# Performance work log

Measured on AMD Instinct MI355X. Metric: run time of the kernel, lower is better.

## Reference

```python
import jax, jax.numpy as jnp
import numpy as np

NUM_HEADS = 16


def trinity_mask(txt_tok, img_tok):
    """Boolean [N, N] mask, True = attend. Faithful to get_mask(..., 'trinity'):
    - image rows attend block-diagonally within 3 equal image chunks
    - text rows attend to all image tokens and causally to text tokens.
    """
    assert img_tok % 3 == 0, "Invalid text token sizes"
    sit = img_tok // 3
    N = txt_tok + img_tok
    i = jnp.arange(N)[:, None]
    j = jnp.arange(N)[None, :]
    img_img = (i < img_tok) & (j < img_tok) & ((i // sit) == (j // sit))
    txt_img = (i >= img_tok) & (j < img_tok)
    txt_txt = (i >= img_tok) & (j >= img_tok) & (i >= j)
    return img_img | txt_img | txt_txt


def setup_inputs() -> dict:
    key = jax.random.key(0)
    ks = jax.random.split(key, 12)
    B, TXT, IMG = 4, 512, 1536
    N = TXT + IMG
    DQ, DKV = 1024, 1024
    s = lambda d: 1.0 / np.sqrt(d).astype(np.float32)
    return {
        "q": jax.random.normal(ks[0], (B, N, DQ), jnp.float32),
        "kv": jax.random.normal(ks[1], (B, N, DKV), jnp.float32),
        "Wq": jax.random.normal(ks[2], (DQ, DQ), jnp.float32) * s(DQ),
        "bq": jnp.zeros((DQ,), jnp.float32),
        "Wk": jax.random.normal(ks[3], (DKV, DQ), jnp.float32) * s(DKV),
        "bk": jnp.zeros((DQ,), jnp.float32),
        "Wv": jax.random.normal(ks[4], (DKV, DQ), jnp.float32) * s(DKV),
        "bv": jnp.zeros((DQ,), jnp.float32),
        "Wo": jax.random.normal(ks[5], (DQ, DQ), jnp.float32) * s(DQ),
        "bo": jnp.zeros((DQ,), jnp.float32),
        "txt_tok_len": TXT,
        "img_tok_len": IMG,
    }


def reference(q, kv, Wq, bq, Wk, bk, Wv, bv, Wo, bo, txt_tok_len, img_tok_len):
    B, N, C = q.shape
    H = NUM_HEADS
    d = C // H
    scale = d ** -0.5
    # projections, split heads: [B, H, N, d]
    qh = (q @ Wq + bq).reshape(B, N, H, d).transpose(0, 2, 1, 3)
    kh = (kv @ Wk + bk).reshape(B, N, H, d).transpose(0, 2, 1, 3)
    vh = (kv @ Wv + bv).reshape(B, N, H, d).transpose(0, 2, 1, 3)
    scores = jnp.einsum("bhqd,bhkd->bhqk", qh, kh) * scale
    mask = trinity_mask(txt_tok_len, img_tok_len)  # [N, N] bool
    scores = jnp.where(mask[None, None], scores, -jnp.inf)
    attn = jax.nn.softmax(scores, axis=-1)
    # dropout in eval mode -> identity
    out = jnp.einsum("bhqk,bhkd->bhqd", attn, vh)
    out = out.transpose(0, 2, 1, 3).reshape(B, N, C)
    return out @ Wo + bo
```

## Files before the change

kernel.cpp:

```cpp
#include <hip/hip_runtime.h>


typedef _Float16 h16;
typedef _Float16 f16x8 __attribute__((ext_vector_type(8)));
typedef __fp16 fp16v2 __attribute__((ext_vector_type(2)));
typedef float f32x4 __attribute__((ext_vector_type(4)));

#define BATCH 4
#define NTOK  2048
#define CDIM  1024
#define NHEAD 16
#define HDIM  64
#define IMGTOK 1536
#define MROWS (BATCH * NTOK)
#define QSCALE 0.18033688011112042f

__device__ __forceinline__ void gload_lds16(const void* g, void* l) {
  __builtin_amdgcn_global_load_lds(
      (const __attribute__((address_space(1))) unsigned int*)g,
      (__attribute__((address_space(3))) unsigned int*)l, 16, 0, 0);
}

__global__ __launch_bounds__(256)
void cvt_f16(const float* __restrict__ s, h16* __restrict__ d) {
  size_t i = ((size_t)blockIdx.x * 256 + threadIdx.x) * 8;
  float4 a = *(const float4*)(s + i);
  float4 b = *(const float4*)(s + i + 4);
  f16x8 o;
  o[0] = (h16)a.x; o[1] = (h16)a.y; o[2] = (h16)a.z; o[3] = (h16)a.w;
  o[4] = (h16)b.x; o[5] = (h16)b.y; o[6] = (h16)b.z; o[7] = (h16)b.w;
  *(f16x8*)(d + i) = o;
}

__global__ __launch_bounds__(256)
void wtrans(const float* __restrict__ W0, const float* __restrict__ W1,
            const float* __restrict__ W2, const float* __restrict__ W3,
            h16* __restrict__ T0, h16* __restrict__ T1,
            h16* __restrict__ T2, h16* __restrict__ T3) {
  const float* W; h16* T;
  switch (blockIdx.z) {
    case 0: W = W0; T = T0; break;
    case 1: W = W1; T = T1; break;
    case 2: W = W2; T = T2; break;
    default: W = W3; T = T3; break;
  }
  __shared__ float t[32][33];
  const int n0 = blockIdx.x * 32, k0 = blockIdx.y * 32;
  const int tx = threadIdx.x, ty = threadIdx.y;
#pragma unroll
  for (int i = 0; i < 4; i++)
    t[ty + 8 * i][tx] = W[(size_t)(k0 + ty + 8 * i) * CDIM + n0 + tx];
  __syncthreads();
#pragma unroll
  for (int i = 0; i < 4; i++)
    T[(size_t)(n0 + ty + 8 * i) * CDIM + k0 + tx] = (h16)t[tx][ty + 8 * i];
}

template <int MODE>
__global__ __launch_bounds__(256, 3)
void gemm_bt(const h16* __restrict__ X, const h16* __restrict__ WT,
             const float* __restrict__ bias, void* __restrict__ outp) {
  __shared__ __attribute__((aligned(16))) h16 smem[3 * 8192];
  const int tid = threadIdx.x;
  const int lane = tid & 63;
  const int w = tid >> 6;
  const int wr = w >> 1, wc = w & 1;
  const int l15 = lane & 15, lhi = lane >> 4;
  const int m0 = blockIdx.y * 128;
  const int n0 = blockIdx.x * 128;

  f32x4 acc[4][4] = {};

  const int sr = tid >> 2;
  const int pc = tid & 3;
  const int lc = pc ^ ((sr >> 1) & 3);
  const h16* gA0 = X + (size_t)(m0 + sr) * CDIM + lc * 8;
  const h16* gA1 = gA0 + (size_t)64 * CDIM;
  const h16* gB0 = WT + (size_t)(n0 + sr) * CDIM + lc * 8;
  const h16* gB1 = gB0 + (size_t)64 * CDIM;

#define GSTAGE(bi, kt)                                      \
  do {                                                      \
    h16* A_ = smem + (bi) * 8192;                           \
    h16* B_ = A_ + 4096;                                    \
    gload_lds16(gA0 + (kt) * 32, A_ + tid * 8);             \
    gload_lds16(gA1 + (kt) * 32, A_ + (256 + tid) * 8);     \
    gload_lds16(gB0 + (kt) * 32, B_ + tid * 8);             \
    gload_lds16(gB1 + (kt) * 32, B_ + (256 + tid) * 8);     \
  } while (0)

  const int NT = CDIM / 32;
  GSTAGE(0, 0);
  GSTAGE(1, 1);
  const int rswz = (l15 >> 1) & 3;

  int rb = 0, sb = 2;
  for (int kt = 0; kt < NT; ++kt) {
    if (kt + 1 < NT) asm volatile("s_waitcnt vmcnt(4)" ::: "memory");
    else             asm volatile("s_waitcnt vmcnt(0)" ::: "memory");
    __builtin_amdgcn_s_barrier();
    if (kt + 2 < NT) { GSTAGE(sb, kt + 2); sb = (sb == 2) ? 0 : sb + 1; }
    const h16* A_ = smem + rb * 8192;
    const h16* B_ = A_ + 4096;
    rb = (rb == 2) ? 0 : rb + 1;
    f16x8 a[4], bb[4];
#pragma unroll
    for (int i = 0; i < 4; i++)
      a[i] = *(const f16x8*)(A_ + (wr * 64 + i * 16 + l15) * 32 + (lhi ^ rswz) * 8);
#pragma unroll
    for (int i = 0; i < 4; i++)
      bb[i] = *(const f16x8*)(B_ + (wc * 64 + i * 16 + l15) * 32 + (lhi ^ rswz) * 8);
    __builtin_amdgcn_s_setprio(1);
#pragma unroll
    for (int i = 0; i < 4; i++)
#pragma unroll
      for (int j = 0; j < 4; j++)
        acc[i][j] = __builtin_amdgcn_mfma_f32_16x16x32_f16(a[i], bb[j], acc[i][j], 0, 0, 0);
    __builtin_amdgcn_s_setprio(0);
  }
#undef GSTAGE

  if constexpr (MODE == 2) {
    __builtin_amdgcn_s_barrier();
    h16* T = smem;
#pragma unroll
    for (int j = 0; j < 4; j++) {
      const int gcL = wc * 64 + j * 16 + l15;
      const float bval = bias[n0 + gcL];
#pragma unroll
      for (int i = 0; i < 4; i++) {
#pragma unroll
        for (int r = 0; r < 4; r++) {
          const int grL = wr * 64 + i * 16 + lhi * 4 + r;
          const int ch = (grL >> 3) ^ (gcL & 15);
          T[gcL * 128 + ch * 8 + (grL & 7)] = (h16)(acc[i][j][r] + bval);
        }
      }
    }
    __builtin_amdgcn_s_barrier();
    const int bsel = m0 >> 11;
    const int nbase = m0 & (NTOK - 1);
    h16* outh = (h16*)outp;
#pragma unroll
    for (int pass = 0; pass < 8; ++pass) {
      const int rowL = pass * 16 + (tid >> 4);
      const int c = tid & 15;
      const int gc = n0 + rowL;
      const int hh = gc >> 6, dd = gc & 63;
      f16x8 v = *(const f16x8*)(T + rowL * 128 + ((c ^ (rowL & 15)) * 8));
      *(f16x8*)(outh + (((size_t)(bsel * NHEAD + hh)) * HDIM + dd) * NTOK +
                nbase + c * 8) = v;
    }
    return;
  }

#pragma unroll
  for (int j = 0; j < 4; j++) {
    const int gc = n0 + wc * 64 + j * 16 + l15;
    const float bval = bias[gc];
#pragma unroll
    for (int i = 0; i < 4; i++) {
      const int grb = m0 + wr * 64 + i * 16 + lhi * 4;
#pragma unroll
      for (int r = 0; r < 4; r++) {
        float v = acc[i][j][r] + bval;
        if constexpr (MODE == 3) v *= QSCALE;
        const int gr = grb + r;
        if constexpr (MODE == 0) {
          ((float*)outp)[(size_t)gr * CDIM + gc] = v;
        } else {
          const int bidx = gr >> 11, n = gr & (NTOK - 1);
          const int hh = gc >> 6, dd = gc & 63;
          ((h16*)outp)[(((size_t)(bidx * NHEAD + hh)) * NTOK + n) * HDIM + dd] = (h16)v;
        }
      }
    }
  }
}

__global__ __launch_bounds__(256)
void attn_kernel(const h16* __restrict__ Qh, const h16* __restrict__ Kh,
                 const h16* __restrict__ VTh, h16* __restrict__ AX) {
  __shared__ __attribute__((aligned(16))) h16 Kb[2][64 * 64];
  __shared__ __attribute__((aligned(16))) h16 Vb[2][64 * 64];
  __shared__ __attribute__((aligned(16))) h16 Pl[4][16 * 64];

  const int tid = threadIdx.x;
  const int lane = tid & 63;
  const int w = tid >> 6;
  const int l15 = lane & 15, lhi = lane >> 4;
  const int lhi4 = lhi * 4;

  const int id = blockIdx.x;
  const int pos = id >> 3;
  const int bh = (id & 7) * 8 + (pos >> 5);
  const int qblk = 31 - (pos & 31);
  const int b = bh >> 4, h = bh & 15;
  const int q0 = qblk * 64;

  const h16* qbase = Qh + (size_t)bh * NTOK * HDIM;
  const h16* kbase = Kh + (size_t)bh * NTOK * HDIM;
  const h16* vbase = VTh + (size_t)bh * HDIM * NTOK;

  const int qrow = q0 + w * 16 + l15;
  const f16x8 qf0 = *(const f16x8*)(qbase + (size_t)qrow * HDIM + lhi * 8);
  const f16x8 qf1 = *(const f16x8*)(qbase + (size_t)qrow * HDIM + 32 + lhi * 8);
  const int qg = qrow;

  const bool is_img = (q0 < IMGTOK);
  int kstart, kend;
  if (is_img) { kstart = q0 & ~511; kend = kstart + 512; }
  else        { kstart = 0;         kend = q0 + 64; }
  const int nt = (kend - kstart) >> 6;

  float m = -3.0e38f, lp = 0.f;
  f32x4 o[4] = {};

  const int srow = tid >> 3;
  const int scc = (tid & 7) ^ (srow & 7);
#define ASTAGE(bufi, k0s)                                                     \
  do {                                                                        \
    gload_lds16(kbase + (size_t)((k0s) + srow) * HDIM + scc * 8,              \
                Kb[bufi] + tid * 8);                                          \
    gload_lds16(kbase + (size_t)((k0s) + 32 + srow) * HDIM + scc * 8,         \
                Kb[bufi] + (256 + tid) * 8);                                  \
    gload_lds16(vbase + (size_t)srow * NTOK + (k0s) + scc * 8,                \
                Vb[bufi] + tid * 8);                                          \
    gload_lds16(vbase + (size_t)(32 + srow) * NTOK + (k0s) + scc * 8,         \
                Vb[bufi] + (256 + tid) * 8);                                  \
  } while (0)

  h16* pl = &Pl[w][0];
  const int x0 = (lhi ^ (l15 & 7)) * 8;
  const int x1 = ((lhi + 4) ^ (l15 & 7)) * 8;
  const int pswz = l15 & 7;
  const int phalf = (lhi & 1) * 4;
  const int plhi2 = lhi >> 1;
  h16* prb = pl + l15 * 64;

  ASTAGE(0, kstart);
  asm volatile("s_waitcnt vmcnt(0)" ::: "memory");
  __builtin_amdgcn_s_barrier();
  int cur = 0;

  for (int t = 0; t < nt; ++t) {
    const int k0 = kstart + t * 64;
    if (t + 1 < nt) ASTAGE(cur ^ 1, kstart + (t + 1) * 64);

    const h16* Kc = Kb[cur];
    f32x4 s[4];
    __builtin_amdgcn_s_setprio(1);
#pragma unroll
    for (int hk = 0; hk < 4; ++hk) {
      const h16* kr = Kc + (hk * 16 + l15) * 64;
      const f16x8 kfa = *(const f16x8*)(kr + x0);
      const f16x8 kfb = *(const f16x8*)(kr + x1);
      f32x4 acc = {};
      acc = __builtin_amdgcn_mfma_f32_16x16x32_f16(kfa, qf0, acc, 0, 0, 0);
      acc = __builtin_amdgcn_mfma_f32_16x16x32_f16(kfb, qf1, acc, 0, 0, 0);
      s[hk] = acc;
    }
    __builtin_amdgcn_s_setprio(0);

    const bool need_mask = (!is_img) && (k0 + 63 >= IMGTOK);
    float sv[4][4];
    float lmax = -3.0e38f;
#pragma unroll
    for (int hk = 0; hk < 4; ++hk) {
#pragma unroll
      for (int r = 0; r < 4; ++r) {
        float v = s[hk][r];
        if (need_mask) {
          const int kg = k0 + hk * 16 + lhi4 + r;
          if (kg >= IMGTOK && kg > qg) v = -1e30f;
        }
        sv[hk][r] = v;
        lmax = fmaxf(lmax, v);
      }
    }
    if (__any(lmax > m + 8.0f)) {
      float vmax = fmaxf(lmax, __shfl_xor(lmax, 16));
      vmax = fmaxf(vmax, __shfl_xor(vmax, 32));
      const float mnew = fmaxf(m, vmax);
      const float corr = exp2f(m - mnew);
      m = mnew;
      lp *= corr;
      const float c0 = __shfl(corr, lhi4 + 0);
      const float c1 = __shfl(corr, lhi4 + 1);
      const float c2 = __shfl(corr, lhi4 + 2);
      const float c3 = __shfl(corr, lhi4 + 3);
#pragma unroll
      for (int dt = 0; dt < 4; dt++) {
        o[dt][0] *= c0; o[dt][1] *= c1; o[dt][2] *= c2; o[dt][3] *= c3;
      }
    }
#pragma unroll
    for (int hk = 0; hk < 4; ++hk) {
      const float e0 = exp2f(sv[hk][0] - m);
      const float e1 = exp2f(sv[hk][1] - m);
      const float e2 = exp2f(sv[hk][2] - m);
      const float e3 = exp2f(sv[hk][3] - m);
      lp += (e0 + e1) + (e2 + e3);
      const fp16v2 lo2 = __builtin_amdgcn_cvt_pkrtz(e0, e1);
      const fp16v2 hi2 = __builtin_amdgcn_cvt_pkrtz(e2, e3);
      uint2 qw;
      qw.x = __builtin_bit_cast(unsigned int, lo2);
      qw.y = __builtin_bit_cast(unsigned int, hi2);
      *(uint2*)(prb + ((hk * 2 + plhi2) ^ pswz) * 8 + phalf) = qw;
    }
    asm volatile("s_waitcnt lgkmcnt(0)" ::: "memory");
    __builtin_amdgcn_sched_barrier(0);

    const h16* Vc = Vb[cur];
    const f16x8 pf0 = *(const f16x8*)(pl + l15 * 64 + x0);
    const f16x8 pf1 = *(const f16x8*)(pl + l15 * 64 + x1);
    __builtin_amdgcn_s_setprio(1);
#pragma unroll
    for (int dt = 0; dt < 4; dt++) {
      const h16* vr = Vc + (dt * 16 + l15) * 64;
      const f16x8 vfa = *(const f16x8*)(vr + x0);
      const f16x8 vfb = *(const f16x8*)(vr + x1);
      o[dt] = __builtin_amdgcn_mfma_f32_16x16x32_f16(pf0, vfa, o[dt], 0, 0, 0);
      o[dt] = __builtin_amdgcn_mfma_f32_16x16x32_f16(pf1, vfb, o[dt], 0, 0, 0);
    }
    __builtin_amdgcn_s_setprio(0);

    asm volatile("s_waitcnt vmcnt(0)" ::: "memory");
    __builtin_amdgcn_s_barrier();
    cur ^= 1;
  }
#undef ASTAGE

  float l = lp;
  l += __shfl_xor(l, 16);
  l += __shfl_xor(l, 32);
  const int qg0 = q0 + w * 16 + lhi4;
#pragma unroll
  for (int r = 0; r < 4; r++) {
    const float lr = __shfl(l, lhi4 + r);
    const float inv = 1.0f / lr;
    const size_t row = (size_t)(b * NTOK + qg0 + r);
#pragma unroll
    for (int dt = 0; dt < 4; dt++) {
      const int col = h * 64 + dt * 16 + l15;
      AX[row * CDIM + col] = (h16)(o[dt][r] * inv);
    }
  }
}

extern "C" void kernel_launch(void* const* d_in, const int* in_sizes, int n_in,
                              void* d_out, int out_size, void* d_ws, size_t ws_size,
                              hipStream_t stream) {
  (void)in_sizes; (void)n_in; (void)out_size; (void)ws_size;
  const float* q  = (const float*)d_in[0];
  const float* kv = (const float*)d_in[1];
  const float* Wq = (const float*)d_in[2];
  const float* bq = (const float*)d_in[3];
  const float* Wk = (const float*)d_in[4];
  const float* bk = (const float*)d_in[5];
  const float* Wv = (const float*)d_in[6];
  const float* bv = (const float*)d_in[7];
  const float* Wo = (const float*)d_in[8];
  const float* bo = (const float*)d_in[9];
  float* out = (float*)d_out;

  char* ws = (char*)d_ws;
  const size_t SZ_MK = (size_t)MROWS * CDIM * sizeof(h16);
  const size_t SZ_W  = (size_t)CDIM * CDIM * sizeof(h16);
  h16* qb  = (h16*)(ws);
  h16* kvb = (h16*)(ws + SZ_MK);
  h16* wqt = (h16*)(ws + 2 * SZ_MK);
  h16* wkt = (h16*)(ws + 2 * SZ_MK + SZ_W);
  h16* wvt = (h16*)(ws + 2 * SZ_MK + 2 * SZ_W);
  h16* wot = (h16*)(ws + 2 * SZ_MK + 3 * SZ_W);
  h16* Qh  = (h16*)(ws + 2 * SZ_MK + 4 * SZ_W);
  h16* Kh  = (h16*)(ws + 3 * SZ_MK + 4 * SZ_W);
  h16* VTh = (h16*)(ws + 4 * SZ_MK + 4 * SZ_W);
  h16* ax  = (h16*)(ws);

  cvt_f16<<<4096, 256, 0, stream>>>(q, qb);
  cvt_f16<<<4096, 256, 0, stream>>>(kv, kvb);
  wtrans<<<dim3(32, 32, 4), dim3(32, 8), 0, stream>>>(Wq, Wk, Wv, Wo,
                                                      wqt, wkt, wvt, wot);
  gemm_bt<3><<<dim3(8, 64), 256, 0, stream>>>(qb, wqt, bq, (void*)Qh);
  gemm_bt<1><<<dim3(8, 64), 256, 0, stream>>>(kvb, wkt, bk, (void*)Kh);
  gemm_bt<2><<<dim3(8, 64), 256, 0, stream>>>(kvb, wvt, bv, (void*)VTh);
  attn_kernel<<<2048, 256, 0, stream>>>(Qh, Kh, VTh, ax);
  gemm_bt<0><<<dim3(8, 64), 256, 0, stream>>>(ax, wot, bo, (void*)out);
}
```

Baseline: 329.1 us.

## Merge QKV projections into one launch and widen attention blocks to 128 queries

```diff
diff --git a/kernel.cpp b/kernel.cpp
--- a/kernel.cpp
+++ b/kernel.cpp
@@ -56,18 +56,31 @@
     T[(size_t)(n0 + ty + 8 * i) * CDIM + k0 + tx] = (h16)t[tx][ty + 8 * i];
 }
 
-template <int MODE>
+
 __global__ __launch_bounds__(256, 3)
-void gemm_bt(const h16* __restrict__ X, const h16* __restrict__ WT,
-             const float* __restrict__ bias, void* __restrict__ outp) {
+void gemm_qkv(const h16* __restrict__ qb, const h16* __restrict__ kvb,
+              const h16* __restrict__ wqt, const h16* __restrict__ wkt,
+              const h16* __restrict__ wvt,
+              const float* __restrict__ bq, const float* __restrict__ bk,
+              const float* __restrict__ bv,
+              h16* __restrict__ Qh, h16* __restrict__ Kh,
+              h16* __restrict__ VTh) {
   __shared__ __attribute__((aligned(16))) h16 smem[3 * 8192];
+  const int id = blockIdx.x;
+  const int gid = (id & 7) * 192 + (id >> 3);
+  const int which = gid >> 9;
+  const int lid = gid & 511;
+  const int m0 = (lid >> 3) * 128;
+  const int n0 = (lid & 7) * 128;
+  const h16* X  = (which == 0) ? qb : kvb;
+  const h16* WT = (which == 0) ? wqt : ((which == 1) ? wkt : wvt);
+  const float* bias = (which == 0) ? bq : ((which == 1) ? bk : bv);
+
   const int tid = threadIdx.x;
   const int lane = tid & 63;
   const int w = tid >> 6;
   const int wr = w >> 1, wc = w & 1;
   const int l15 = lane & 15, lhi = lane >> 4;
-  const int m0 = blockIdx.y * 128;
-  const int n0 = blockIdx.x * 128;
 
   f32x4 acc[4][4] = {};
 
@@ -120,7 +133,7 @@
   }
 #undef GSTAGE
 
-  if constexpr (MODE == 2) {
+  if (which == 2) {
     __builtin_amdgcn_s_barrier();
     h16* T = smem;
 #pragma unroll
@@ -140,7 +153,6 @@
     __builtin_amdgcn_s_barrier();
     const int bsel = m0 >> 11;
     const int nbase = m0 & (NTOK - 1);
-    h16* outh = (h16*)outp;
 #pragma unroll
     for (int pass = 0; pass < 8; ++pass) {
       const int rowL = pass * 16 + (tid >> 4);
@@ -148,12 +160,14 @@
       const int gc = n0 + rowL;
       const int hh = gc >> 6, dd = gc & 63;
       f16x8 v = *(const f16x8*)(T + rowL * 128 + ((c ^ (rowL & 15)) * 8));
-      *(f16x8*)(outh + (((size_t)(bsel * NHEAD + hh)) * HDIM + dd) * NTOK +
+      *(f16x8*)(VTh + (((size_t)(bsel * NHEAD + hh)) * HDIM + dd) * NTOK +
                 nbase + c * 8) = v;
     }
     return;
   }
 
+  h16* outp = (which == 0) ? Qh : Kh;
+  const float scale = (which == 0) ? QSCALE : 1.0f;
 #pragma unroll
   for (int j = 0; j < 4; j++) {
     const int gc = n0 + wc * 64 + j * 16 + l15;
@@ -163,27 +177,102 @@
       const int grb = m0 + wr * 64 + i * 16 + lhi * 4;
 #pragma unroll
       for (int r = 0; r < 4; r++) {
-        float v = acc[i][j][r] + bval;
-        if constexpr (MODE == 3) v *= QSCALE;
+        const float v = (acc[i][j][r] + bval) * scale;
         const int gr = grb + r;
-        if constexpr (MODE == 0) {
-          ((float*)outp)[(size_t)gr * CDIM + gc] = v;
-        } else {
-          const int bidx = gr >> 11, n = gr & (NTOK - 1);
-          const int hh = gc >> 6, dd = gc & 63;
-          ((h16*)outp)[(((size_t)(bidx * NHEAD + hh)) * NTOK + n) * HDIM + dd] = (h16)v;
-        }
+        const int bidx = gr >> 11, n = gr & (NTOK - 1);
+        const int hh = gc >> 6, dd = gc & 63;
+        outp[(((size_t)(bidx * NHEAD + hh)) * NTOK + n) * HDIM + dd] = (h16)v;
       }
     }
   }
 }
 
-__global__ __launch_bounds__(256)
+__global__ __launch_bounds__(256, 3)
+void gemm_out(const h16* __restrict__ X, const h16* __restrict__ WT,
+              const float* __restrict__ bias, float* __restrict__ outp) {
+  __shared__ __attribute__((aligned(16))) h16 smem[3 * 8192];
+  const int id = blockIdx.x;
+  const int gid = (id & 7) * 64 + (id >> 3);
+  const int m0 = (gid >> 3) * 128;
+  const int n0 = (gid & 7) * 128;
+
+  const int tid = threadIdx.x;
+  const int lane = tid & 63;
+  const int w = tid >> 6;
+  const int wr = w >> 1, wc = w & 1;
+  const int l15 = lane & 15, lhi = lane >> 4;
+
+  f32x4 acc[4][4] = {};
+
+  const int sr = tid >> 2;
+  const int pc = tid & 3;
+  const int lc = pc ^ ((sr >> 1) & 3);
+  const h16* gA0 = X + (size_t)(m0 + sr) * CDIM + lc * 8;
+  const h16* gA1 = gA0 + (size_t)64 * CDIM;
+  const h16* gB0 = WT + (size_t)(n0 + sr) * CDIM + lc * 8;
+  const h16* gB1 = gB0 + (size_t)64 * CDIM;
+
+#define GSTAGE(bi, kt)                                      \
+  do {                                                      \
+    h16* A_ = smem + (bi) * 8192;                           \
+    h16* B_ = A_ + 4096;                                    \
+    gload_lds16(gA0 + (kt) * 32, A_ + tid * 8);             \
+    gload_lds16(gA1 + (kt) * 32, A_ + (256 + tid) * 8);     \
+    gload_lds16(gB0 + (kt) * 32, B_ + tid * 8);             \
+    gload_lds16(gB1 + (kt) * 32, B_ + (256 + tid) * 8);     \
+  } while (0)
+
+  const int NT = CDIM / 32;
+  GSTAGE(0, 0);
+  GSTAGE(1, 1);
+  const int rswz = (l15 >> 1) & 3;
+
+  int rb = 0, sb = 2;
+  for (int kt = 0; kt < NT; ++kt) {
+    if (kt + 1 < NT) asm volatile("s_waitcnt vmcnt(4)" ::: "memory");
+    else             asm volatile("s_waitcnt vmcnt(0)" ::: "memory");
+    __builtin_amdgcn_s_barrier();
+    if (kt + 2 < NT) { GSTAGE(sb, kt + 2); sb = (sb == 2) ? 0 : sb + 1; }
+    const h16* A_ = smem + rb * 8192;
+    const h16* B_ = A_ + 4096;
+    rb = (rb == 2) ? 0 : rb + 1;
+    f16x8 a[4], bb[4];
+#pragma unroll
+    for (int i = 0; i < 4; i++)
+      a[i] = *(const f16x8*)(A_ + (wr * 64 + i * 16 + l15) * 32 + (lhi ^ rswz) * 8);
+#pragma unroll
+    for (int i = 0; i < 4; i++)
+      bb[i] = *(const f16x8*)(B_ + (wc * 64 + i * 16 + l15) * 32 + (lhi ^ rswz) * 8);
+    __builtin_amdgcn_s_setprio(1);
+#pragma unroll
+    for (int i = 0; i < 4; i++)
+#pragma unroll
+      for (int j = 0; j < 4; j++)
+        acc[i][j] = __builtin_amdgcn_mfma_f32_16x16x32_f16(a[i], bb[j], acc[i][j], 0, 0, 0);
+    __builtin_amdgcn_s_setprio(0);
+  }
+#undef GSTAGE
+
+#pragma unroll
+  for (int j = 0; j < 4; j++) {
+    const int gc = n0 + wc * 64 + j * 16 + l15;
+    const float bval = bias[gc];
+#pragma unroll
+    for (int i = 0; i < 4; i++) {
+      const int grb = m0 + wr * 64 + i * 16 + lhi * 4;
+#pragma unroll
+      for (int r = 0; r < 4; r++)
+        outp[(size_t)(grb + r) * CDIM + gc] = acc[i][j][r] + bval;
+    }
+  }
+}
+
+__global__ __launch_bounds__(512, 6)
 void attn_kernel(const h16* __restrict__ Qh, const h16* __restrict__ Kh,
                  const h16* __restrict__ VTh, h16* __restrict__ AX) {
   __shared__ __attribute__((aligned(16))) h16 Kb[2][64 * 64];
   __shared__ __attribute__((aligned(16))) h16 Vb[2][64 * 64];
-  __shared__ __attribute__((aligned(16))) h16 Pl[4][16 * 64];
+  __shared__ __attribute__((aligned(16))) h16 Pl[8][16 * 64];
 
   const int tid = threadIdx.x;
   const int lane = tid & 63;
@@ -193,10 +282,10 @@
 
   const int id = blockIdx.x;
   const int pos = id >> 3;
-  const int bh = (id & 7) * 8 + (pos >> 5);
-  const int qblk = 31 - (pos & 31);
+  const int bh = (id & 7) * 8 + (pos >> 4);
+  const int qblk = 15 - (pos & 15);
   const int b = bh >> 4, h = bh & 15;
-  const int q0 = qblk * 64;
+  const int q0 = qblk * 128;
 
   const h16* qbase = Qh + (size_t)bh * NTOK * HDIM;
   const h16* kbase = Kh + (size_t)bh * NTOK * HDIM;
@@ -208,9 +297,8 @@
   const int qg = qrow;
 
   const bool is_img = (q0 < IMGTOK);
-  int kstart, kend;
-  if (is_img) { kstart = q0 & ~511; kend = kstart + 512; }
-  else        { kstart = 0;         kend = q0 + 64; }
+  const int kstart = is_img ? (q0 & ~511) : 0;
+  const int kend = is_img ? (kstart + 512) : (q0 + 128);
   const int nt = (kend - kstart) >> 6;
 
   float m = -3.0e38f, lp = 0.f;
@@ -222,12 +310,8 @@
   do {                                                                        \
     gload_lds16(kbase + (size_t)((k0s) + srow) * HDIM + scc * 8,              \
                 Kb[bufi] + tid * 8);                                          \
-    gload_lds16(kbase + (size_t)((k0s) + 32 + srow) * HDIM + scc * 8,         \
-                Kb[bufi] + (256 + tid) * 8);                                  \
     gload_lds16(vbase + (size_t)srow * NTOK + (k0s) + scc * 8,                \
                 Vb[bufi] + tid * 8);                                          \
-    gload_lds16(vbase + (size_t)(32 + srow) * NTOK + (k0s) + scc * 8,         \
-                Vb[bufi] + (256 + tid) * 8);                                  \
   } while (0)
 
   h16* pl = &Pl[w][0];
@@ -245,7 +329,7 @@
 
   for (int t = 0; t < nt; ++t) {
     const int k0 = kstart + t * 64;
-    if (t + 1 < nt) ASTAGE(cur ^ 1, kstart + (t + 1) * 64);
+    if (t + 1 < nt) ASTAGE(cur ^ 1, k0 + 64);
 
     const h16* Kc = Kb[cur];
     f32x4 s[4];
@@ -262,22 +346,30 @@
     }
     __builtin_amdgcn_s_setprio(0);
 
+    const h16* Vc = Vb[cur];
+    const h16* vr0 = Vc + l15 * 64;
+    const h16* vr1 = Vc + (16 + l15) * 64;
+    const f16x8 va0 = *(const f16x8*)(vr0 + x0);
+    const f16x8 vb0 = *(const f16x8*)(vr0 + x1);
+    const f16x8 va1 = *(const f16x8*)(vr1 + x0);
+    const f16x8 vb1 = *(const f16x8*)(vr1 + x1);
+
     const bool need_mask = (!is_img) && (k0 + 63 >= IMGTOK);
-    float sv[4][4];
+    if (need_mask) {
+#pragma unroll
+      for (int hk = 0; hk < 4; ++hk)
+#pragma unroll
+        for (int r = 0; r < 4; ++r) {
+          const int kg = k0 + hk * 16 + lhi4 + r;
+          if (kg >= IMGTOK && kg > qg) s[hk][r] = -1e30f;
+        }
+    }
     float lmax = -3.0e38f;
 #pragma unroll
-    for (int hk = 0; hk < 4; ++hk) {
-#pragma unroll
-      for (int r = 0; r < 4; ++r) {
-        float v = s[hk][r];
-        if (need_mask) {
-          const int kg = k0 + hk * 16 + lhi4 + r;
-          if (kg >= IMGTOK && kg > qg) v = -1e30f;
-        }
-        sv[hk][r] = v;
-        lmax = fmaxf(lmax, v);
-      }
-    }
+    for (int hk = 0; hk < 4; ++hk)
+#pragma unroll
+      for (int r = 0; r < 4; ++r) lmax = fmaxf(lmax, s[hk][r]);
+
     if (__any(lmax > m + 8.0f)) {
       float vmax = fmaxf(lmax, __shfl_xor(lmax, 16));
       vmax = fmaxf(vmax, __shfl_xor(vmax, 32));
@@ -296,10 +388,10 @@
     }
 #pragma unroll
     for (int hk = 0; hk < 4; ++hk) {
-      const float e0 = exp2f(sv[hk][0] - m);
-      const float e1 = exp2f(sv[hk][1] - m);
-      const float e2 = exp2f(sv[hk][2] - m);
-      const float e3 = exp2f(sv[hk][3] - m);
+      const float e0 = exp2f(s[hk][0] - m);
+      const float e1 = exp2f(s[hk][1] - m);
+      const float e2 = exp2f(s[hk][2] - m);
+      const float e3 = exp2f(s[hk][3] - m);
       lp += (e0 + e1) + (e2 + e3);
       const fp16v2 lo2 = __builtin_amdgcn_cvt_pkrtz(e0, e1);
       const fp16v2 hi2 = __builtin_amdgcn_cvt_pkrtz(e2, e3);
@@ -308,21 +400,27 @@
       qw.y = __builtin_bit_cast(unsigned int, hi2);
       *(uint2*)(prb + ((hk * 2 + plhi2) ^ pswz) * 8 + phalf) = qw;
     }
+
+    const h16* vr2 = Vc + (32 + l15) * 64;
+    const h16* vr3 = Vc + (48 + l15) * 64;
+    const f16x8 va2 = *(const f16x8*)(vr2 + x0);
+    const f16x8 vb2 = *(const f16x8*)(vr2 + x1);
+    const f16x8 va3 = *(const f16x8*)(vr3 + x0);
+    const f16x8 vb3 = *(const f16x8*)(vr3 + x1);
+    const f16x8 pf0 = *(const f16x8*)(pl + l15 * 64 + x0);
+    const f16x8 pf1 = *(const f16x8*)(pl + l15 * 64 + x1);
     asm volatile("s_waitcnt lgkmcnt(0)" ::: "memory");
     __builtin_amdgcn_sched_barrier(0);
 
-    const h16* Vc = Vb[cur];
-    const f16x8 pf0 = *(const f16x8*)(pl + l15 * 64 + x0);
-    const f16x8 pf1 = *(const f16x8*)(pl + l15 * 64 + x1);
     __builtin_amdgcn_s_setprio(1);
-#pragma unroll
-    for (int dt = 0; dt < 4; dt++) {
-      const h16* vr = Vc + (dt * 16 + l15) * 64;
-      const f16x8 vfa = *(const f16x8*)(vr + x0);
-      const f16x8 vfb = *(const f16x8*)(vr + x1);
-      o[dt] = __builtin_amdgcn_mfma_f32_16x16x32_f16(pf0, vfa, o[dt], 0, 0, 0);
-      o[dt] = __builtin_amdgcn_mfma_f32_16x16x32_f16(pf1, vfb, o[dt], 0, 0, 0);
-    }
+    o[0] = __builtin_amdgcn_mfma_f32_16x16x32_f16(pf0, va0, o[0], 0, 0, 0);
+    o[0] = __builtin_amdgcn_mfma_f32_16x16x32_f16(pf1, vb0, o[0], 0, 0, 0);
+    o[1] = __builtin_amdgcn_mfma_f32_16x16x32_f16(pf0, va1, o[1], 0, 0, 0);
+    o[1] = __builtin_amdgcn_mfma_f32_16x16x32_f16(pf1, vb1, o[1], 0, 0, 0);
+    o[2] = __builtin_amdgcn_mfma_f32_16x16x32_f16(pf0, va2, o[2], 0, 0, 0);
+    o[2] = __builtin_amdgcn_mfma_f32_16x16x32_f16(pf1, vb2, o[2], 0, 0, 0);
+    o[3] = __builtin_amdgcn_mfma_f32_16x16x32_f16(pf0, va3, o[3], 0, 0, 0);
+    o[3] = __builtin_amdgcn_mfma_f32_16x16x32_f16(pf1, vb3, o[3], 0, 0, 0);
     __builtin_amdgcn_s_setprio(0);
 
     asm volatile("s_waitcnt vmcnt(0)" ::: "memory");
@@ -382,9 +480,8 @@
   cvt_f16<<<4096, 256, 0, stream>>>(kv, kvb);
   wtrans<<<dim3(32, 32, 4), dim3(32, 8), 0, stream>>>(Wq, Wk, Wv, Wo,
                                                       wqt, wkt, wvt, wot);
-  gemm_bt<3><<<dim3(8, 64), 256, 0, stream>>>(qb, wqt, bq, (void*)Qh);
-  gemm_bt<1><<<dim3(8, 64), 256, 0, stream>>>(kvb, wkt, bk, (void*)Kh);
-  gemm_bt<2><<<dim3(8, 64), 256, 0, stream>>>(kvb, wvt, bv, (void*)VTh);
-  attn_kernel<<<2048, 256, 0, stream>>>(Qh, Kh, VTh, ax);
-  gemm_bt<0><<<dim3(8, 64), 256, 0, stream>>>(ax, wot, bo, (void*)out);
-}
+  gemm_qkv<<<1536, 256, 0, stream>>>(qb, kvb, wqt, wkt, wvt, bq, bk, bv,
+                                     Qh, Kh, VTh);
+  attn_kernel<<<1024, 512, 0, stream>>>(Qh, Kh, VTh, ax);
+  gemm_out<<<512, 256, 0, stream>>>(ax, wot, bo, out);
+}
```

Measured after the change: 372.9 us. 1.13x slower.
